# Optimization experiments

Hardware: AMD Instinct MI355X
Metric: run time of the kernel (lower is better)

Reference implementation:

```python
import jax, jax.numpy as jnp
import numpy as np

N, F = 12288, 512
NEG_INF = jnp.float32(-1e9)  # matches Keras BaseDenseAttention mask additive constant


def setup_inputs() -> dict:
    key = jax.random.key(0)
    k1, k2 = jax.random.split(key)
    features = jax.random.normal(k1, (N, F), dtype=jnp.float32)
    A = jax.random.randint(k2, (N, N), 0, 2).astype(jnp.int32)
    return {"features": features, "A": A}


def reference(features, A):
    # Keras Attention with query=key=value=dropout(features); dropout is identity
    # at inference. use_scale=False -> plain dot-product scores, no 1/sqrt(d).
    scores = jnp.einsum("nf,mf->nm", features, features)          # [N, N]
    scores = jnp.where(A > 0, scores, NEG_INF)                    # mask non-edges
    attn = jax.nn.softmax(scores, axis=-1)                        # softmax over keys
    return jnp.einsum("nm,mf->nf", attn, features)                # [N, F]
```

## Files before the change

kernel.cpp:

```cpp
#include <hip/hip_runtime.h>
#include <cstddef>
#include <cstdint>

#define NN 12288
#define FF 512
#define NWORDS (NN / 32)
#define NKT (NN / 128)

using half8 = __attribute__((ext_vector_type(8))) _Float16;
using half4 = __attribute__((ext_vector_type(4))) _Float16;
using f32x4 = __attribute__((ext_vector_type(4))) float;

constexpr float MASK_NEG = -1e9f;

__device__ __forceinline__ void gll16(const void* g, void* l) {
    __builtin_amdgcn_global_load_lds((const __attribute__((address_space(1))) void*)g,
                                     (__attribute__((address_space(3))) void*)l, 16, 0, 0);
}

__global__ __launch_bounds__(256)
void compress_mask_kernel(const int* __restrict__ Amat, uint32_t* __restrict__ Abits) {
    const size_t W = (size_t)blockIdx.x * blockDim.x + threadIdx.x;
    const int4* p = reinterpret_cast<const int4*>(Amat + W * 32);
    uint32_t b = 0;
#pragma unroll
    for (int q = 0; q < 8; ++q) {
        const int4 v = p[q];
        b |= (uint32_t)(v.x > 0) << (4 * q + 0);
        b |= (uint32_t)(v.y > 0) << (4 * q + 1);
        b |= (uint32_t)(v.z > 0) << (4 * q + 2);
        b |= (uint32_t)(v.w > 0) << (4 * q + 3);
    }
    Abits[W] = b;
}

__global__ void cvt_feat_kernel(const float* __restrict__ in, _Float16* __restrict__ out) {
    const size_t i = ((size_t)blockIdx.x * blockDim.x + threadIdx.x) * 8;
    float4 x = *reinterpret_cast<const float4*>(in + i);
    float4 y = *reinterpret_cast<const float4*>(in + i + 4);
    half8 h;
    h[0] = (_Float16)x.x; h[1] = (_Float16)x.y; h[2] = (_Float16)x.z; h[3] = (_Float16)x.w;
    h[4] = (_Float16)y.x; h[5] = (_Float16)y.y; h[6] = (_Float16)y.z; h[7] = (_Float16)y.w;
    *reinterpret_cast<half8*>(out + i) = h;
}

__global__ void transpose_feat_kernel(const float* __restrict__ in, _Float16* __restrict__ outT) {
    __shared__ float tile[32][33];
    const int bi = blockIdx.x;
    const int bj = blockIdx.y;
    const int r  = threadIdx.x >> 3;
    const int c4 = (threadIdx.x & 7) << 2;
    float4 v = *reinterpret_cast<const float4*>(in + (size_t)(bi * 32 + r) * FF + bj * 32 + c4);
    tile[r][c4 + 0] = v.x; tile[r][c4 + 1] = v.y; tile[r][c4 + 2] = v.z; tile[r][c4 + 3] = v.w;
    __syncthreads();
    half4 h;
#pragma unroll
    for (int k = 0; k < 4; ++k) h[k] = (_Float16)tile[c4 + k][r];
    *reinterpret_cast<half4*>(outT + (size_t)(bj * 32 + r) * NN + bi * 32 + c4) = h;
}

__global__ __launch_bounds__(256)
void gemm1_exp(const _Float16* __restrict__ feath, const uint32_t* __restrict__ Abits,
               _Float16* __restrict__ Pmat, float* __restrict__ m_t, _Float16* __restrict__ s_t) {
    __shared__ alignas(16) _Float16 As[2][128 * 32];
    __shared__ alignas(16) _Float16 Bs[2][128 * 32];
    __shared__ alignas(16) float rowmax2[128][2];
    __shared__ alignas(16) float rowsum2[128][2];

    const int tid = threadIdx.x, lane = tid & 63, wid = tid >> 6;
    const int g = lane >> 4, a = lane & 15;
    const int wr = wid >> 1, wc = wid & 1;
    const int row0 = blockIdx.x * 128, col0 = blockIdx.y * 128;

    f32x4 acc[4][4];
#pragma unroll
    for (int i = 0; i < 4; ++i)
#pragma unroll
        for (int j = 0; j < 4; ++j) acc[i][j] = f32x4{0.f, 0.f, 0.f, 0.f};

    const int lr = lane >> 2;
    const int li = (lane & 3) * 8;

    auto stage = [&](int buf, int t) {
#pragma unroll
        for (int c = 0; c < 2; ++c) {
            const int ch = wid * 2 + c;
            gll16(feath + (size_t)(row0 + ch * 16 + lr) * FF + t * 32 + li, &As[buf][ch * 512]);
            gll16(feath + (size_t)(col0 + ch * 16 + lr) * FF + t * 32 + li, &Bs[buf][ch * 512]);
        }
    };

    stage(0, 0);
    __syncthreads();
    int buf = 0;
    for (int t = 0; t < 16; ++t) {
        if (t + 1 < 16) stage(buf ^ 1, t + 1);
        half8 af[4], bf[4];
#pragma unroll
        for (int rf = 0; rf < 4; ++rf)
            af[rf] = *reinterpret_cast<const half8*>(&As[buf][(64 * wr + 16 * rf + a) * 32 + 8 * g]);
#pragma unroll
        for (int cf = 0; cf < 4; ++cf)
            bf[cf] = *reinterpret_cast<const half8*>(&Bs[buf][(64 * wc + 16 * cf + a) * 32 + 8 * g]);
#pragma unroll
        for (int rf = 0; rf < 4; ++rf)
#pragma unroll
            for (int cf = 0; cf < 4; ++cf)
                acc[rf][cf] = __builtin_amdgcn_mfma_f32_16x16x32_f16(af[rf], bf[cf], acc[rf][cf], 0, 0, 0);
        __syncthreads();
        buf ^= 1;
    }

    const int cw0 = (col0 + 64 * wc) >> 5;
    uint2 am[4][4];
#pragma unroll
    for (int rf = 0; rf < 4; ++rf)
#pragma unroll
        for (int r = 0; r < 4; ++r) {
            const int grow = row0 + 64 * wr + 16 * rf + 4 * g + r;
            am[rf][r] = *reinterpret_cast<const uint2*>(&Abits[(size_t)grow * NWORDS + cw0]);
        }
#pragma unroll
    for (int rf = 0; rf < 4; ++rf)
#pragma unroll
        for (int r = 0; r < 4; ++r) {
#pragma unroll
            for (int cf = 0; cf < 4; ++cf) {
                const uint32_t w = (cf < 2) ? am[rf][r].x : am[rf][r].y;
                const uint32_t bit = (w >> (a + 16 * (cf & 1))) & 1u;
                acc[rf][cf][r] = bit ? acc[rf][cf][r] : MASK_NEG;
            }
        }

#pragma unroll
    for (int rf = 0; rf < 4; ++rf) {
#pragma unroll
        for (int r = 0; r < 4; ++r) {
            float v = fmaxf(fmaxf(acc[rf][0][r], acc[rf][1][r]), fmaxf(acc[rf][2][r], acc[rf][3][r]));
            v = fmaxf(v, __shfl_xor(v, 1, 16));
            v = fmaxf(v, __shfl_xor(v, 2, 16));
            v = fmaxf(v, __shfl_xor(v, 4, 16));
            v = fmaxf(v, __shfl_xor(v, 8, 16));
            if (a == 0) rowmax2[64 * wr + 16 * rf + 4 * g + r][wc] = v;
        }
    }
    __syncthreads();

#pragma unroll
    for (int rf = 0; rf < 4; ++rf) {
#pragma unroll
        for (int r = 0; r < 4; ++r) {
            const int lrow = 64 * wr + 16 * rf + 4 * g + r;
            const float mt = fmaxf(rowmax2[lrow][0], rowmax2[lrow][1]);
            const size_t rbase = (size_t)(row0 + lrow) * NN + col0 + 64 * wc + a;
            float ps = 0.f;
#pragma unroll
            for (int cf = 0; cf < 4; ++cf) {
                const float p = __expf(acc[rf][cf][r] - mt);
                ps += p;
                Pmat[rbase + 16 * cf] = (_Float16)p;
            }
            ps += __shfl_xor(ps, 1, 16);
            ps += __shfl_xor(ps, 2, 16);
            ps += __shfl_xor(ps, 4, 16);
            ps += __shfl_xor(ps, 8, 16);
            if (a == 0) rowsum2[lrow][wc] = ps;
        }
    }
    __syncthreads();
    if (tid < 128) {
        m_t[(size_t)blockIdx.y * NN + row0 + tid] = fmaxf(rowmax2[tid][0], rowmax2[tid][1]);
        s_t[(size_t)blockIdx.y * NN + row0 + tid] = (_Float16)(rowsum2[tid][0] + rowsum2[tid][1]);
    }
}

__global__ __launch_bounds__(256)
void stats_kernel(const float* __restrict__ m_t, const _Float16* __restrict__ s_t,
                  _Float16* __restrict__ sc_t, float* __restrict__ l_row) {
    const int r = blockIdx.x * 256 + threadIdx.x;
    float m = -3.0e38f;
#pragma unroll 4
    for (int kt = 0; kt < NKT; ++kt) m = fmaxf(m, m_t[(size_t)kt * NN + r]);
    float l = 0.f;
#pragma unroll 4
    for (int kt = 0; kt < NKT; ++kt) {
        const float e = __expf(m_t[(size_t)kt * NN + r] - m);
        sc_t[(size_t)kt * NN + r] = (_Float16)e;
        l += e * (float)s_t[(size_t)kt * NN + r];
    }
    l_row[r] = l;
}

__global__ __launch_bounds__(256)
void gemm2_scale(const _Float16* __restrict__ Pmat, const _Float16* __restrict__ featT,
                 const _Float16* __restrict__ sc_t, const float* __restrict__ l_row,
                 float* __restrict__ out) {
    __shared__ alignas(16) _Float16 As[2][128 * 32];
    __shared__ alignas(16) _Float16 Bs[2][128 * 32];

    const int tid = threadIdx.x, lane = tid & 63, wid = tid >> 6;
    const int g = lane >> 4, a = lane & 15;
    const int wr = wid >> 1, wc = wid & 1;
    const int col0 = blockIdx.x * 128, row0 = blockIdx.y * 128;

    f32x4 acc[4][4];
#pragma unroll
    for (int i = 0; i < 4; ++i)
#pragma unroll
        for (int j = 0; j < 4; ++j) acc[i][j] = f32x4{0.f, 0.f, 0.f, 0.f};

    const int lr = lane >> 2;
    const int li = (lane & 3) * 8;

    auto stage = [&](int buf, int t) {
#pragma unroll
        for (int c = 0; c < 2; ++c) {
            const int ch = wid * 2 + c;
            gll16(Pmat  + (size_t)(row0 + ch * 16 + lr) * NN + t * 32 + li, &As[buf][ch * 512]);
            gll16(featT + (size_t)(col0 + ch * 16 + lr) * NN + t * 32 + li, &Bs[buf][ch * 512]);
        }
    };

    stage(0, 0);
    __syncthreads();
    int buf = 0;
    _Float16 sc[4] = {(_Float16)1.f, (_Float16)1.f, (_Float16)1.f, (_Float16)1.f};
    for (int t = 0; t < 384; ++t) {
        if ((t & 3) == 0) {
            const int kt = t >> 2;
#pragma unroll
            for (int rf = 0; rf < 4; ++rf)
                sc[rf] = sc_t[(size_t)kt * NN + row0 + 64 * wr + 16 * rf + a];
        }
        if (t + 1 < 384) stage(buf ^ 1, t + 1);
        half8 af[4], bf[4];
#pragma unroll
        for (int rf = 0; rf < 4; ++rf) {
            af[rf] = *reinterpret_cast<const half8*>(&As[buf][(64 * wr + 16 * rf + a) * 32 + 8 * g]);
            af[rf] = af[rf] * sc[rf];
        }
#pragma unroll
        for (int cf = 0; cf < 4; ++cf)
            bf[cf] = *reinterpret_cast<const half8*>(&Bs[buf][(64 * wc + 16 * cf + a) * 32 + 8 * g]);
#pragma unroll
        for (int rf = 0; rf < 4; ++rf)
#pragma unroll
            for (int cf = 0; cf < 4; ++cf)
                acc[rf][cf] = __builtin_amdgcn_mfma_f32_16x16x32_f16(af[rf], bf[cf], acc[rf][cf], 0, 0, 0);
        __syncthreads();
        buf ^= 1;
    }

#pragma unroll
    for (int rf = 0; rf < 4; ++rf) {
#pragma unroll
        for (int r = 0; r < 4; ++r) {
            const int grow = row0 + 64 * wr + 16 * rf + 4 * g + r;
            const float il = 1.0f / l_row[grow];
#pragma unroll
            for (int cf = 0; cf < 4; ++cf) {
                const int gcol = col0 + 64 * wc + 16 * cf + a;
                out[(size_t)grow * FF + gcol] = acc[rf][cf][r] * il;
            }
        }
    }
}

constexpr int BM_ = 64;
constexpr int BN_ = 64;
constexpr int KV_STRIDE = 520;

template<bool RH>
__global__ __launch_bounds__(512, 2)
void attn_flash(const float* __restrict__ featf, const _Float16* __restrict__ feath,
                const int* __restrict__ Amat, float* __restrict__ out) {
    __shared__ alignas(16) _Float16 kv[BN_ * KV_STRIDE];
    __shared__ alignas(16) _Float16 pbuf[BM_][72];
    __shared__ alignas(16) float pmax[BM_][2];
    __shared__ alignas(16) float psum[BM_][2];
    __shared__ alignas(16) float m_s[BM_];
    __shared__ alignas(16) float l_s[BM_];
    __shared__ alignas(16) float rscale[BM_];

    const int tid  = threadIdx.x;
    const int lane = tid & 63;
    const int wid  = tid >> 6;
    const int g    = lane >> 4;
    const int a    = lane & 15;
    const int rg   = wid >> 1;
    const int ch   = wid & 1;
    const int qrow0 = blockIdx.x * BM_;

    half8 qf[16];
    {
        const int qr = qrow0 + 16 * rg + a;
#pragma unroll
        for (int ks = 0; ks < 16; ++ks) {
            const int f0 = 32 * ks + 8 * g;
            if constexpr (RH) {
                qf[ks] = *reinterpret_cast<const half8*>(feath + (size_t)qr * FF + f0);
            } else {
                const float* sp = featf + (size_t)qr * FF + f0;
                float4 x = *reinterpret_cast<const float4*>(sp);
                float4 y = *reinterpret_cast<const float4*>(sp + 4);
                half8 h;
                h[0] = (_Float16)x.x; h[1] = (_Float16)x.y; h[2] = (_Float16)x.z; h[3] = (_Float16)x.w;
                h[4] = (_Float16)y.x; h[5] = (_Float16)y.y; h[6] = (_Float16)y.z; h[7] = (_Float16)y.w;
                qf[ks] = h;
            }
        }
    }

    f32x4 acc[4][4];
#pragma unroll
    for (int i = 0; i < 4; ++i)
#pragma unroll
        for (int j = 0; j < 4; ++j) acc[i][j] = f32x4{0.f, 0.f, 0.f, 0.f};

    if (tid < BM_) { m_s[tid] = -INFINITY; l_s[tid] = 0.f; }
    __syncthreads();

    for (int kt = 0; kt < NN / BN_; ++kt) {
        const int key0 = kt * BN_;
#pragma unroll
        for (int i = 0; i < 8; ++i) {
            const int flat8 = tid + i * 512;
            const int key   = flat8 >> 6;
            const int b     = flat8 & 63;
            const int slot  = (b + (key >> 3)) & 63;
            _Float16* dst = &kv[key * KV_STRIDE + slot * 8];
            if constexpr (RH) {
                *reinterpret_cast<half8*>(dst) =
                    *reinterpret_cast<const half8*>(feath + (size_t)(key0 + key) * FF + b * 8);
            } else {
                const float* sp = featf + (size_t)(key0 + key) * FF + b * 8;
                float4 x = *reinterpret_cast<const float4*>(sp);
                float4 y = *reinterpret_cast<const float4*>(sp + 4);
                half8 h;
                h[0] = (_Float16)x.x; h[1] = (_Float16)x.y; h[2] = (_Float16)x.z; h[3] = (_Float16)x.w;
                h[4] = (_Float16)y.x; h[5] = (_Float16)y.y; h[6] = (_Float16)y.z; h[7] = (_Float16)y.w;
                *reinterpret_cast<half8*>(dst) = h;
            }
        }

        int am[2][4];
#pragma unroll
        for (int fc = 0; fc < 2; ++fc)
#pragma unroll
            for (int r = 0; r < 4; ++r) {
                const int arow = qrow0 + 16 * rg + 4 * g + r;
                const int acol = key0 + 32 * ch + 16 * fc + a;
                am[fc][r] = Amat[(size_t)arow * NN + acol];
            }
        __syncthreads();

        f32x4 s0{0.f, 0.f, 0.f, 0.f}, s1{0.f, 0.f, 0.f, 0.f};
        const int bk0 = 32 * ch + a;
        const int bk1 = bk0 + 16;
        const int kb0 = bk0 >> 3;
        const int kb1 = bk1 >> 3;
        const _Float16* kr0 = &kv[bk0 * KV_STRIDE];
        const _Float16* kr1 = &kv[bk1 * KV_STRIDE];
#pragma unroll
        for (int ks = 0; ks < 16; ++ks) {
            const int b = 4 * ks + g;
            const half8 bf0 = *reinterpret_cast<const half8*>(kr0 + (((b + kb0) & 63) << 3));
            const half8 bf1 = *reinterpret_cast<const half8*>(kr1 + (((b + kb1) & 63) << 3));
            s0 = __builtin_amdgcn_mfma_f32_16x16x32_f16(qf[ks], bf0, s0, 0, 0, 0);
            s1 = __builtin_amdgcn_mfma_f32_16x16x32_f16(qf[ks], bf1, s1, 0, 0, 0);
        }

        float sv[2][4];
#pragma unroll
        for (int r = 0; r < 4; ++r) {
            sv[0][r] = (am[0][r] > 0) ? s0[r] : MASK_NEG;
            sv[1][r] = (am[1][r] > 0) ? s1[r] : MASK_NEG;
        }
#pragma unroll
        for (int r = 0; r < 4; ++r) {
            float v = fmaxf(sv[0][r], sv[1][r]);
            v = fmaxf(v, __shfl_xor(v, 1, 16));
            v = fmaxf(v, __shfl_xor(v, 2, 16));
            v = fmaxf(v, __shfl_xor(v, 4, 16));
            v = fmaxf(v, __shfl_xor(v, 8, 16));
            if (a == 0) pmax[16 * rg + 4 * g + r][ch] = v;
        }
        __syncthreads();

#pragma unroll
        for (int r = 0; r < 4; ++r) {
            const int row = 16 * rg + 4 * g + r;
            const float mo = m_s[row];
            const float mn = fmaxf(mo, fmaxf(pmax[row][0], pmax[row][1]));
            const float p0 = __expf(sv[0][r] - mn);
            const float p1 = __expf(sv[1][r] - mn);
            pbuf[row][32 * ch + a]      = (_Float16)p0;
            pbuf[row][32 * ch + 16 + a] = (_Float16)p1;
            float ssum = p0 + p1;
            ssum += __shfl_xor(ssum, 1, 16);
            ssum += __shfl_xor(ssum, 2, 16);
            ssum += __shfl_xor(ssum, 4, 16);
            ssum += __shfl_xor(ssum, 8, 16);
            if (a == 0) psum[row][ch] = ssum;
        }
        __syncthreads();

        if (tid < BM_) {
            const float mo = m_s[tid];
            const float mn = fmaxf(mo, fmaxf(pmax[tid][0], pmax[tid][1]));
            const float sc = __expf(mo - mn);
            l_s[tid] = l_s[tid] * sc + psum[tid][0] + psum[tid][1];
            m_s[tid] = mn;
            rscale[tid] = sc;
        }
        __syncthreads();

#pragma unroll
        for (int rf = 0; rf < 4; ++rf) {
            const float4 scv = *reinterpret_cast<const float4*>(&rscale[16 * rf + 4 * g]);
#pragma unroll
            for (int cf = 0; cf < 4; ++cf) {
                acc[rf][cf][0] *= scv.x; acc[rf][cf][1] *= scv.y;
                acc[rf][cf][2] *= scv.z; acc[rf][cf][3] *= scv.w;
            }
        }
#pragma unroll
        for (int kk = 0; kk < 2; ++kk) {
            half8 af[4];
#pragma unroll
            for (int rf = 0; rf < 4; ++rf)
                af[rf] = *reinterpret_cast<const half8*>(&pbuf[16 * rf + a][32 * kk + 8 * g]);
            const int keybase = 32 * kk + 8 * g;
#pragma unroll
            for (int cf = 0; cf < 4; ++cf) {
                const int col  = 64 * wid + 16 * cf + a;
                const int slot = (((col >> 3) + 4 * kk + g) & 63);
                const _Float16* vb = &kv[(size_t)keybase * KV_STRIDE + (slot << 3) + (col & 7)];
                half8 bf;
#pragma unroll
                for (int j = 0; j < 8; ++j)
                    bf[j] = vb[j * KV_STRIDE];
#pragma unroll
                for (int rf = 0; rf < 4; ++rf)
                    acc[rf][cf] = __builtin_amdgcn_mfma_f32_16x16x32_f16(af[rf], bf, acc[rf][cf], 0, 0, 0);
            }
        }
        __syncthreads();
    }

#pragma unroll
    for (int rf = 0; rf < 4; ++rf) {
        const float4 lv = *reinterpret_cast<const float4*>(&l_s[16 * rf + 4 * g]);
        const float inv[4] = {1.f / lv.x, 1.f / lv.y, 1.f / lv.z, 1.f / lv.w};
#pragma unroll
        for (int cf = 0; cf < 4; ++cf) {
            const int col = 64 * wid + 16 * cf + a;
#pragma unroll
            for (int r = 0; r < 4; ++r) {
                out[(size_t)(qrow0 + 16 * rf + 4 * g + r) * FF + col] = acc[rf][cf][r] * inv[r];
            }
        }
    }
}

extern "C" void kernel_launch(void* const* d_in, const int* in_sizes, int n_in,
                              void* d_out, int out_size, void* d_ws, size_t ws_size,
                              hipStream_t stream) {
    const float* features = (const float*)d_in[0];
    const int*   Amat     = (const int*)d_in[1];
    float*       out      = (float*)d_out;

    const size_t P_bytes   = (size_t)NN * NN * 2;
    const size_t f16_bytes = (size_t)NN * FF * 2;
    const size_t sct_bytes = (size_t)NKT * NN * 2;
    const size_t st_bytes  = (size_t)NKT * NN * 2;
    const size_t l_bytes   = (size_t)NN * 4;
    const size_t total     = P_bytes + 2 * f16_bytes + sct_bytes + st_bytes + l_bytes;

    if (ws_size >= total) {
        char* w = (char*)d_ws;
        _Float16* Pmat  = (_Float16*)w;   w += P_bytes;
        _Float16* feath = (_Float16*)w;   w += f16_bytes;
        _Float16* featT = (_Float16*)w;   w += f16_bytes;
        _Float16* sc_t  = (_Float16*)w;   w += sct_bytes;
        _Float16* s_t   = (_Float16*)w;   w += st_bytes;
        float*    l_row = (float*)w;

        uint32_t* Abits = (uint32_t*)d_out;
        float*    m_t   = (float*)((char*)d_out + (size_t)NN * NWORDS * 4);

        compress_mask_kernel<<<(NN * NWORDS) / 256, 256, 0, stream>>>(Amat, Abits);
        cvt_feat_kernel<<<(NN * FF) / (256 * 8), 256, 0, stream>>>(features, feath);
        transpose_feat_kernel<<<dim3(NN / 32, FF / 32), 256, 0, stream>>>(features, featT);
        gemm1_exp<<<dim3(NN / 128, NN / 128), 256, 0, stream>>>(feath, Abits, Pmat, m_t, s_t);
        stats_kernel<<<NN / 256, 256, 0, stream>>>(m_t, s_t, sc_t, l_row);
        gemm2_scale<<<dim3(FF / 128, NN / 128), 256, 0, stream>>>(Pmat, featT, sc_t, l_row, out);
    } else if (ws_size >= f16_bytes) {
        _Float16* feath = (_Float16*)d_ws;
        cvt_feat_kernel<<<(NN * FF) / (256 * 8), 256, 0, stream>>>(features, feath);
        attn_flash<true><<<NN / BM_, 512, 0, stream>>>(features, feath, Amat, out);
    } else {
        attn_flash<false><<<NN / BM_, 512, 0, stream>>>(features, nullptr, Amat, out);
    }
}
```

Before: 894.4 us.

## Drop mask compression pass, fuse feature prep, retile gemm2 to 128x64

Removes the separate mask bit-packing kernel. gemm1 now reads the int32 adjacency entries directly, prefetching them into a 64-bit register mask before the GEMM loop so the latency overlaps compute. It also merges the fp16 convert and transpose kernels into one pass over features. gemm2 moves to 128x64 tiles, doubling its block count for better CU occupancy, and prefetches the per-tile softmax scale factors one k-tile ahead. The trade-off is that gemm1 reads 4-byte mask values instead of bits with less coalesced access, and the smaller gemm2 tiles re-read the P matrix twice as often.

Measured after the change: 938.7 us. 1.05x slower.

```diff
diff --git a/kernel.cpp b/kernel.cpp
--- a/kernel.cpp
+++ b/kernel.cpp
@@ -4,7 +4,6 @@
 
 #define NN 12288
 #define FF 512
-#define NWORDS (NN / 32)
 #define NKT (NN / 128)
 
 using half8 = __attribute__((ext_vector_type(8))) _Float16;
@@ -19,19 +18,23 @@
 }
 
 __global__ __launch_bounds__(256)
-void compress_mask_kernel(const int* __restrict__ Amat, uint32_t* __restrict__ Abits) {
-    const size_t W = (size_t)blockIdx.x * blockDim.x + threadIdx.x;
-    const int4* p = reinterpret_cast<const int4*>(Amat + W * 32);
-    uint32_t b = 0;
-#pragma unroll
-    for (int q = 0; q < 8; ++q) {
-        const int4 v = p[q];
-        b |= (uint32_t)(v.x > 0) << (4 * q + 0);
-        b |= (uint32_t)(v.y > 0) << (4 * q + 1);
-        b |= (uint32_t)(v.z > 0) << (4 * q + 2);
-        b |= (uint32_t)(v.w > 0) << (4 * q + 3);
-    }
-    Abits[W] = b;
+void prep_feat_kernel(const float* __restrict__ in, _Float16* __restrict__ feath,
+                      _Float16* __restrict__ featT) {
+    __shared__ float tile[32][33];
+    const int bi = blockIdx.x;
+    const int bj = blockIdx.y;
+    const int r  = threadIdx.x >> 3;
+    const int c4 = (threadIdx.x & 7) << 2;
+    float4 v = *reinterpret_cast<const float4*>(in + (size_t)(bi * 32 + r) * FF + bj * 32 + c4);
+    tile[r][c4 + 0] = v.x; tile[r][c4 + 1] = v.y; tile[r][c4 + 2] = v.z; tile[r][c4 + 3] = v.w;
+    half4 hr;
+    hr[0] = (_Float16)v.x; hr[1] = (_Float16)v.y; hr[2] = (_Float16)v.z; hr[3] = (_Float16)v.w;
+    *reinterpret_cast<half4*>(feath + (size_t)(bi * 32 + r) * FF + bj * 32 + c4) = hr;
+    __syncthreads();
+    half4 h;
+#pragma unroll
+    for (int k = 0; k < 4; ++k) h[k] = (_Float16)tile[c4 + k][r];
+    *reinterpret_cast<half4*>(featT + (size_t)(bj * 32 + r) * NN + bi * 32 + c4) = h;
 }
 
 __global__ void cvt_feat_kernel(const float* __restrict__ in, _Float16* __restrict__ out) {
@@ -44,23 +47,8 @@
     *reinterpret_cast<half8*>(out + i) = h;
 }
 
-__global__ void transpose_feat_kernel(const float* __restrict__ in, _Float16* __restrict__ outT) {
-    __shared__ float tile[32][33];
-    const int bi = blockIdx.x;
-    const int bj = blockIdx.y;
-    const int r  = threadIdx.x >> 3;
-    const int c4 = (threadIdx.x & 7) << 2;
-    float4 v = *reinterpret_cast<const float4*>(in + (size_t)(bi * 32 + r) * FF + bj * 32 + c4);
-    tile[r][c4 + 0] = v.x; tile[r][c4 + 1] = v.y; tile[r][c4 + 2] = v.z; tile[r][c4 + 3] = v.w;
-    __syncthreads();
-    half4 h;
-#pragma unroll
-    for (int k = 0; k < 4; ++k) h[k] = (_Float16)tile[c4 + k][r];
-    *reinterpret_cast<half4*>(outT + (size_t)(bj * 32 + r) * NN + bi * 32 + c4) = h;
-}
-
 __global__ __launch_bounds__(256)
-void gemm1_exp(const _Float16* __restrict__ feath, const uint32_t* __restrict__ Abits,
+void gemm1_exp(const _Float16* __restrict__ feath, const int* __restrict__ Amat,
                _Float16* __restrict__ Pmat, float* __restrict__ m_t, _Float16* __restrict__ s_t) {
     __shared__ alignas(16) _Float16 As[2][128 * 32];
     __shared__ alignas(16) _Float16 Bs[2][128 * 32];
@@ -90,6 +78,19 @@
         }
     };
 
+    unsigned long long bits = 0ULL;
+#pragma unroll
+    for (int rf = 0; rf < 4; ++rf)
+#pragma unroll
+        for (int r = 0; r < 4; ++r) {
+            const size_t rb = (size_t)(row0 + 64 * wr + 16 * rf + 4 * g + r) * NN + col0 + 64 * wc + a;
+#pragma unroll
+            for (int cf = 0; cf < 4; ++cf) {
+                const int v = Amat[rb + 16 * cf];
+                bits |= (unsigned long long)(v > 0) << (rf * 16 + r * 4 + cf);
+            }
+        }
+
     stage(0, 0);
     __syncthreads();
     int buf = 0;
@@ -111,29 +112,18 @@
         buf ^= 1;
     }
 
-    const int cw0 = (col0 + 64 * wc) >> 5;
-    uint2 am[4][4];
 #pragma unroll
     for (int rf = 0; rf < 4; ++rf)
 #pragma unroll
-        for (int r = 0; r < 4; ++r) {
-            const int grow = row0 + 64 * wr + 16 * rf + 4 * g + r;
-            am[rf][r] = *reinterpret_cast<const uint2*>(&Abits[(size_t)grow * NWORDS + cw0]);
-        }
+        for (int r = 0; r < 4; ++r)
+#pragma unroll
+            for (int cf = 0; cf < 4; ++cf) {
+                const unsigned long long bit = (bits >> (rf * 16 + r * 4 + cf)) & 1ULL;
+                acc[rf][cf][r] = bit ? acc[rf][cf][r] : MASK_NEG;
+            }
+
 #pragma unroll
     for (int rf = 0; rf < 4; ++rf)
-#pragma unroll
-        for (int r = 0; r < 4; ++r) {
-#pragma unroll
-            for (int cf = 0; cf < 4; ++cf) {
-                const uint32_t w = (cf < 2) ? am[rf][r].x : am[rf][r].y;
-                const uint32_t bit = (w >> (a + 16 * (cf & 1))) & 1u;
-                acc[rf][cf][r] = bit ? acc[rf][cf][r] : MASK_NEG;
-            }
-        }
-
-#pragma unroll
-    for (int rf = 0; rf < 4; ++rf) {
 #pragma unroll
         for (int r = 0; r < 4; ++r) {
             float v = fmaxf(fmaxf(acc[rf][0][r], acc[rf][1][r]), fmaxf(acc[rf][2][r], acc[rf][3][r]));
@@ -143,11 +133,10 @@
             v = fmaxf(v, __shfl_xor(v, 8, 16));
             if (a == 0) rowmax2[64 * wr + 16 * rf + 4 * g + r][wc] = v;
         }
-    }
-    __syncthreads();
-
-#pragma unroll
-    for (int rf = 0; rf < 4; ++rf) {
+    __syncthreads();
+
+#pragma unroll
+    for (int rf = 0; rf < 4; ++rf)
 #pragma unroll
         for (int r = 0; r < 4; ++r) {
             const int lrow = 64 * wr + 16 * rf + 4 * g + r;
@@ -166,7 +155,6 @@
             ps += __shfl_xor(ps, 8, 16);
             if (a == 0) rowsum2[lrow][wc] = ps;
         }
-    }
     __syncthreads();
     if (tid < 128) {
         m_t[(size_t)blockIdx.y * NN + row0 + tid] = fmaxf(rowmax2[tid][0], rowmax2[tid][1]);
@@ -196,74 +184,79 @@
                  const _Float16* __restrict__ sc_t, const float* __restrict__ l_row,
                  float* __restrict__ out) {
     __shared__ alignas(16) _Float16 As[2][128 * 32];
-    __shared__ alignas(16) _Float16 Bs[2][128 * 32];
+    __shared__ alignas(16) _Float16 Bs[2][64 * 32];
 
     const int tid = threadIdx.x, lane = tid & 63, wid = tid >> 6;
     const int g = lane >> 4, a = lane & 15;
     const int wr = wid >> 1, wc = wid & 1;
-    const int col0 = blockIdx.x * 128, row0 = blockIdx.y * 128;
-
-    f32x4 acc[4][4];
-#pragma unroll
-    for (int i = 0; i < 4; ++i)
-#pragma unroll
-        for (int j = 0; j < 4; ++j) acc[i][j] = f32x4{0.f, 0.f, 0.f, 0.f};
+    const int col0 = blockIdx.x * 64, row0 = blockIdx.y * 128;
+
+    f32x4 acc[4][2];
+#pragma unroll
+    for (int i = 0; i < 4; ++i) { acc[i][0] = f32x4{0.f,0.f,0.f,0.f}; acc[i][1] = f32x4{0.f,0.f,0.f,0.f}; }
 
     const int lr = lane >> 2;
     const int li = (lane & 3) * 8;
+    const size_t scbase = row0 + 64 * wr + a;
 
     auto stage = [&](int buf, int t) {
 #pragma unroll
         for (int c = 0; c < 2; ++c) {
             const int ch = wid * 2 + c;
-            gll16(Pmat  + (size_t)(row0 + ch * 16 + lr) * NN + t * 32 + li, &As[buf][ch * 512]);
-            gll16(featT + (size_t)(col0 + ch * 16 + lr) * NN + t * 32 + li, &Bs[buf][ch * 512]);
-        }
+            gll16(Pmat + (size_t)(row0 + ch * 16 + lr) * NN + t * 32 + li, &As[buf][ch * 512]);
+        }
+        gll16(featT + (size_t)(col0 + wid * 16 + lr) * NN + t * 32 + li, &Bs[buf][wid * 512]);
     };
 
+    _Float16 pend[4], sc[4];
+#pragma unroll
+    for (int rf = 0; rf < 4; ++rf) pend[rf] = sc_t[scbase + 16 * rf];
+
     stage(0, 0);
     __syncthreads();
     int buf = 0;
-    _Float16 sc[4] = {(_Float16)1.f, (_Float16)1.f, (_Float16)1.f, (_Float16)1.f};
     for (int t = 0; t < 384; ++t) {
         if ((t & 3) == 0) {
-            const int kt = t >> 2;
-#pragma unroll
-            for (int rf = 0; rf < 4; ++rf)
-                sc[rf] = sc_t[(size_t)kt * NN + row0 + 64 * wr + 16 * rf + a];
+#pragma unroll
+            for (int rf = 0; rf < 4; ++rf) sc[rf] = pend[rf];
+            const int ktn = (t >> 2) + 1;
+            if (ktn < NKT) {
+#pragma unroll
+                for (int rf = 0; rf < 4; ++rf)
+                    pend[rf] = sc_t[(size_t)ktn * NN + scbase + 16 * rf];
+            }
         }
         if (t + 1 < 384) stage(buf ^ 1, t + 1);
-        half8 af[4], bf[4];
+        half8 af[4], bf[2];
 #pragma unroll
         for (int rf = 0; rf < 4; ++rf) {
             af[rf] = *reinterpret_cast<const half8*>(&As[buf][(64 * wr + 16 * rf + a) * 32 + 8 * g]);
             af[rf] = af[rf] * sc[rf];
         }
 #pragma unroll
-        for (int cf = 0; cf < 4; ++cf)
-            bf[cf] = *reinterpret_cast<const half8*>(&Bs[buf][(64 * wc + 16 * cf + a) * 32 + 8 * g]);
+        for (int cf = 0; cf < 2; ++cf)
+            bf[cf] = *reinterpret_cast<const half8*>(&Bs[buf][(32 * wc + 16 * cf + a) * 32 + 8 * g]);
 #pragma unroll
         for (int rf = 0; rf < 4; ++rf)
 #pragma unroll
-            for (int cf = 0; cf < 4; ++cf)
+            for (int cf = 0; cf < 2; ++cf)
                 acc[rf][cf] = __builtin_amdgcn_mfma_f32_16x16x32_f16(af[rf], bf[cf], acc[rf][cf], 0, 0, 0);
         __syncthreads();
         buf ^= 1;
     }
 
 #pragma unroll
-    for (int rf = 0; rf < 4; ++rf) {
+    for (int rf = 0; rf < 4; ++rf)
 #pragma unroll
         for (int r = 0; r < 4; ++r) {
             const int grow = row0 + 64 * wr + 16 * rf + 4 * g + r;
             const float il = 1.0f / l_row[grow];
 #pragma unroll
-            for (int cf = 0; cf < 4; ++cf) {
-                const int gcol = col0 + 64 * wc + 16 * cf + a;
+            for (int cf = 0; cf < 2; ++cf) {
+                const int gcol = col0 + 32 * wc + 16 * cf + a;
                 out[(size_t)grow * FF + gcol] = acc[rf][cf][r] * il;
             }
         }
-    }
 }
 
 constexpr int BM_ = 64;
@@ -486,15 +479,12 @@
         _Float16* s_t   = (_Float16*)w;   w += st_bytes;
         float*    l_row = (float*)w;
 
-        uint32_t* Abits = (uint32_t*)d_out;
-        float*    m_t   = (float*)((char*)d_out + (size_t)NN * NWORDS * 4);
-
-        compress_mask_kernel<<<(NN * NWORDS) / 256, 256, 0, stream>>>(Amat, Abits);
-        cvt_feat_kernel<<<(NN * FF) / (256 * 8), 256, 0, stream>>>(features, feath);
-        transpose_feat_kernel<<<dim3(NN / 32, FF / 32), 256, 0, stream>>>(features, featT);
-        gemm1_exp<<<dim3(NN / 128, NN / 128), 256, 0, stream>>>(feath, Abits, Pmat, m_t, s_t);
+        float* m_t = (float*)d_out;
+
+        prep_feat_kernel<<<dim3(NN / 32, FF / 32), 256, 0, stream>>>(features, feath, featT);
+        gemm1_exp<<<dim3(NN / 128, NN / 128), 256, 0, stream>>>(feath, Amat, Pmat, m_t, s_t);
         stats_kernel<<<NN / 256, 256, 0, stream>>>(m_t, s_t, sc_t, l_row);
-        gemm2_scale<<<dim3(FF / 128, NN / 128), 256, 0, stream>>>(Pmat, featT, sc_t, l_row, out);
+        gemm2_scale<<<dim3(FF / 64, NN / 128), 256, 0, stream>>>(Pmat, featT, sc_t, l_row, out);
     } else if (ws_size >= f16_bytes) {
         _Float16* feath = (_Float16*)d_ws;
         cvt_feat_kernel<<<(NN * FF) / (256 * 8), 256, 0, stream>>>(features, feath);
```
